# Kernel optimization log

Measured on AMD Instinct MI355X. Metric: run time of the kernel, lower is better.

Reference implementation:

```python
import jax, jax.numpy as jnp
import numpy as np

N = 20000          # nodes
E = 320000         # directed edges (self-loops added in reference)
F_IN = 128         # input node features
HEADS = 8
HID = 64           # per-head hidden channels
G = 64             # graphs in the batch
NUM_CLASSES = 10
NEG_SLOPE = 0.2    # PyG GATConv LeakyReLU slope


def _gat_layer(x, src, dst, W, a_src, a_dst, bias, n_nodes):
    """PyG-style GATConv: messages flow src->dst, softmax over incoming edges."""
    H, C = a_src.shape
    h = (x @ W).reshape(n_nodes, H, C)                     # [N,H,C]
    asrc = jnp.einsum('nhc,hc->nh', h, a_src)              # [N,H]
    adst = jnp.einsum('nhc,hc->nh', h, a_dst)              # [N,H]
    e = jax.nn.leaky_relu(asrc[src] + adst[dst], NEG_SLOPE)  # [Etot,H]
    emax = jax.ops.segment_max(e, dst, num_segments=n_nodes)  # [N,H]
    ee = jnp.exp(e - emax[dst])
    denom = jax.ops.segment_sum(ee, dst, num_segments=n_nodes)
    alpha = ee / (denom[dst] + 1e-16)                      # [Etot,H]
    out = jax.ops.segment_sum(h[src] * alpha[:, :, None], dst, num_segments=n_nodes)
    return out.reshape(n_nodes, H * C) + bias


def setup_inputs() -> dict:
    key = jax.random.key(0)
    ks = jax.random.split(key, 10)
    x = jax.random.normal(ks[0], (N, F_IN), jnp.float32)
    edge_index = jax.random.randint(ks[1], (2, E), 0, N, jnp.int32)
    batch = jnp.sort(jax.random.randint(ks[2], (N,), 0, G, jnp.int32))
    # layer 1: F_IN -> HEADS*HID (concat)
    W1 = jax.random.normal(ks[3], (F_IN, HEADS * HID), jnp.float32) / np.float32(np.sqrt(F_IN))
    a_src1 = jax.random.normal(ks[4], (HEADS, HID), jnp.float32) / np.float32(np.sqrt(HID))
    a_dst1 = jax.random.normal(ks[5], (HEADS, HID), jnp.float32) / np.float32(np.sqrt(HID))
    b1 = jnp.zeros((HEADS * HID,), jnp.float32)
    # layer 2: HEADS*HID -> NUM_CLASSES (1 head)
    W2 = jax.random.normal(ks[6], (HEADS * HID, NUM_CLASSES), jnp.float32) / np.float32(np.sqrt(HEADS * HID))
    a_src2 = jax.random.normal(ks[7], (1, NUM_CLASSES), jnp.float32) / np.float32(np.sqrt(NUM_CLASSES))
    a_dst2 = jax.random.normal(ks[8], (1, NUM_CLASSES), jnp.float32) / np.float32(np.sqrt(NUM_CLASSES))
    b2 = jnp.zeros((NUM_CLASSES,), jnp.float32)
    return {"x": x, "edge_index": edge_index, "batch": batch,
            "W1": W1, "a_src1": a_src1, "a_dst1": a_dst1, "b1": b1,
            "W2": W2, "a_src2": a_src2, "a_dst2": a_dst2, "b2": b2}


def reference(x, edge_index, batch, W1, a_src1, a_dst1, b1, W2, a_src2, a_dst2, b2):
    n = x.shape[0]
    loop = jnp.arange(n, dtype=edge_index.dtype)   # add_self_loops=True (PyG default)
    src = jnp.concatenate([edge_index[0], loop])
    dst = jnp.concatenate([edge_index[1], loop])
    h = jax.nn.elu(_gat_layer(x, src, dst, W1, a_src1, a_dst1, b1, n))
    h = _gat_layer(h, src, dst, W2, a_src2, a_dst2, b2, n)
    # PowerMeanAggregation with default p=1.0 == mean pooling per graph
    sums = jax.ops.segment_sum(h, batch, num_segments=G)                    # [G,NC]
    counts = jax.ops.segment_sum(jnp.ones((n, 1), h.dtype), batch, num_segments=G)
    return sums / jnp.maximum(counts, 1.0)
```

## Files before the change

kernel.cpp:

```cpp
#include <hip/hip_runtime.h>
#include <hip/hip_bf16.h>

typedef unsigned short ushort_t;
typedef unsigned int uint_t;

typedef __attribute__((ext_vector_type(8))) short bf16x8;
typedef __attribute__((ext_vector_type(4))) float f32x4;

__device__ __forceinline__ float bf2f(ushort_t u) {
    union { uint_t i; float f; } v; v.i = ((uint_t)u) << 16; return v.f;
}
__device__ __forceinline__ float bits2f(uint_t i) {
    union { uint_t i; float f; } v; v.i = i; return v.f;
}
__device__ __forceinline__ ushort_t f2bf(float f) {
    __hip_bfloat16 h = __float2bfloat16(f);
    ushort_t u; __builtin_memcpy(&u, &h, 2); return u;
}
__device__ __forceinline__ float leaky(float v) { return (v > 0.f) ? v : 0.2f * v; }

#define PO_AS1 0
#define PO_AD1 512
#define PO_B1  1024
#define PO_W2  1536
#define PO_AS2 6656
#define PO_AD2 6666
#define PO_B2  6676
#define PTOT   6686

__device__ __forceinline__ bool detect_fp32_local(const ushort_t* __restrict__ xa) {
    __shared__ int cnt;
    if (threadIdx.x == 0) cnt = 0;
    __syncthreads();
    int bad = 0;
    for (int i = threadIdx.x; i < 4096; i += 256) {
        float v = bf2f(xa[i]);
        if (!(fabsf(v) < 1e4f)) bad++;
    }
    if (bad) atomicAdd(&cnt, bad);
    __syncthreads();
    return cnt >= 16;
}

__global__ __launch_bounds__(256) void k_prep(const void* __restrict__ x,
                                              const void* __restrict__ W1,
                                              const void* as1, const void* ad1,
                                              const void* b1, const void* W2,
                                              const void* as2, const void* ad2,
                                              const void* b2,
                                              ushort_t* __restrict__ W1t,
                                              float* __restrict__ prm,
                                              int* __restrict__ deg, int N) {
    int b = blockIdx.x, t = threadIdx.x;
    if (b < 283) {
        bool isf = detect_fp32_local((const ushort_t*)x);
        if (b < 256) {
            int idx = b * 256 + t;
            int n = idx & 511, k = idx >> 9;
            float v = isf ? ((const float*)W1)[k * 512 + n]
                          : bf2f(((const ushort_t*)W1)[k * 512 + n]);
            W1t[n * 128 + k] = f2bf(v);
        } else {
            int i = (b - 256) * 256 + t;
            if (i < PTOT) {
                const void* src; int off;
                if (i < 512)       { src = as1; off = i; }
                else if (i < 1024) { src = ad1; off = i - 512; }
                else if (i < 1536) { src = b1;  off = i - 1024; }
                else if (i < 6656) { src = W2;  off = i - 1536; }
                else if (i < 6666) { src = as2; off = i - 6656; }
                else if (i < 6676) { src = ad2; off = i - 6666; }
                else               { src = b2;  off = i - 6676; }
                prm[i] = isf ? ((const float*)src)[off] : bf2f(((const ushort_t*)src)[off]);
            }
        }
    } else {
        int i = (b - 283) * 256 + t;
        if (i < N) deg[i] = 0;
    }
}

__global__ __launch_bounds__(256) void k_gemm1(const void* __restrict__ xraw,
                                               const ushort_t* __restrict__ w1t,
                                               const float* __restrict__ prm,
                                               ushort_t* __restrict__ h1,
                                               float* __restrict__ asrcf,
                                               float* __restrict__ adstf) {
    int t = threadIdx.x;
    int wave = t >> 6, lane = t & 63;
    int m0 = blockIdx.x * 16;
    bool isf = detect_fp32_local((const ushort_t*)xraw);
    __shared__ ushort_t sA[16 * 128];
    {
        size_t base = (size_t)m0 * 128;
        for (int i = t; i < 2048; i += 256)
            sA[i] = isf ? f2bf(((const float*)xraw)[base + i])
                        : ((const ushort_t*)xraw)[base + i];
    }
    __syncthreads();
    int mr = lane & 15, quad = lane >> 4;
    int n0 = wave * 128;
    f32x4 acc[8];
#pragma unroll
    for (int ct = 0; ct < 8; ++ct) acc[ct] = {0.f, 0.f, 0.f, 0.f};
#pragma unroll
    for (int kk = 0; kk < 4; ++kk) {
        bf16x8 a = *reinterpret_cast<const bf16x8*>(&sA[mr * 128 + quad * 8 + kk * 32]);
#pragma unroll
        for (int ct = 0; ct < 8; ++ct) {
            bf16x8 bb = *reinterpret_cast<const bf16x8*>(
                &w1t[(size_t)(n0 + ct * 16 + mr) * 128 + quad * 8 + kk * 32]);
            acc[ct] = __builtin_amdgcn_mfma_f32_16x16x32_bf16(a, bb, acc[ct], 0, 0, 0);
        }
    }
    int col = lane & 15;
#pragma unroll
    for (int hh = 0; hh < 2; ++hh) {
        float Ss[4] = {0.f, 0.f, 0.f, 0.f}, Dd[4] = {0.f, 0.f, 0.f, 0.f};
#pragma unroll
        for (int c4 = 0; c4 < 4; ++c4) {
            int ct = hh * 4 + c4;
            int abscol = n0 + ct * 16 + col;
            float asv = prm[PO_AS1 + abscol];
            float adv = prm[PO_AD1 + abscol];
            float ps[4], pd[4];
#pragma unroll
            for (int r = 0; r < 4; ++r) {
                h1[(size_t)(m0 + quad * 4 + r) * 512 + abscol] = f2bf(acc[ct][r]);
                ps[r] = acc[ct][r] * asv;
                pd[r] = acc[ct][r] * adv;
            }
#pragma unroll
            for (int off = 1; off <= 8; off <<= 1) {
#pragma unroll
                for (int r = 0; r < 4; ++r) {
                    ps[r] += __shfl_xor(ps[r], off, 64);
                    pd[r] += __shfl_xor(pd[r], off, 64);
                }
            }
#pragma unroll
            for (int r = 0; r < 4; ++r) { Ss[r] += ps[r]; Dd[r] += pd[r]; }
        }
        if (col == 0) {
            int head = 2 * wave + hh;
#pragma unroll
            for (int r = 0; r < 4; ++r) {
                asrcf[(m0 + quad * 4 + r) * 8 + head] = Ss[r];
                adstf[(m0 + quad * 4 + r) * 8 + head] = Dd[r];
            }
        }
    }
}

__global__ void k_hist(const int* __restrict__ ei, int* __restrict__ deg, int E, int Etot) {
    int e = blockIdx.x * 256 + threadIdx.x;
    if (e >= Etot) return;
    int dst = (e < E) ? ei[E + e] : (e - E);
    atomicAdd(&deg[dst], 1);
}

__global__ __launch_bounds__(1024) void k_scan1(const int* __restrict__ deg,
                                                int* __restrict__ rowptr,
                                                int* __restrict__ bsum, int N) {
    int b = blockIdx.x, t = threadIdx.x;
    int lane = t & 63, wv = t >> 6;
    int i = b * 1000 + t;
    int v = (t < 1000 && i < N) ? deg[i] : 0;
    int sv = v;
#pragma unroll
    for (int off = 1; off < 64; off <<= 1) {
        int u = __shfl_up(sv, off, 64);
        if (lane >= off) sv += u;
    }
    __shared__ int wsum[16], woff[16];
    if (lane == 63) wsum[wv] = sv;
    __syncthreads();
    if (t < 16) {
        int s = wsum[t], sc = s;
#pragma unroll
        for (int off = 1; off < 16; off <<= 1) {
            int u = __shfl_up(sc, off, 16);
            if ((t & 15) >= off) sc += u;
        }
        woff[t] = sc - s;
    }
    __syncthreads();
    int inc = sv + woff[wv];
    if (t < 1000 && i < N) rowptr[i + 1] = inc;
    if (t == 1023) bsum[b] = inc;
}

__global__ __launch_bounds__(64) void k_scan2(const int* __restrict__ bsum,
                                              int* __restrict__ boffs) {
    int l = threadIdx.x;
    int v = (l < 20) ? bsum[l] : 0;
    int sc = v;
#pragma unroll
    for (int off = 1; off < 64; off <<= 1) {
        int u = __shfl_up(sc, off, 64);
        if (l >= off) sc += u;
    }
    if (l < 20) boffs[l] = sc - v;
}

__global__ __launch_bounds__(256) void k_scan3(const int* __restrict__ deg,
                                               const int* __restrict__ boffs,
                                               int* __restrict__ rowptr,
                                               int* __restrict__ cursor, int N) {
    int i = blockIdx.x * 256 + threadIdx.x;
    if (i >= N) return;
    int r = rowptr[i + 1] + boffs[i / 1000];
    rowptr[i + 1] = r;
    cursor[i] = r - deg[i];
    if (i == 0) rowptr[0] = 0;
}

__global__ void k_scatter(const int* __restrict__ ei, int* __restrict__ cursor,
                          int* __restrict__ csr_src, int E, int Etot) {
    int e = blockIdx.x * 256 + threadIdx.x;
    if (e >= Etot) return;
    int src, dst;
    if (e < E) { src = ei[e]; dst = ei[E + e]; } else { src = dst = e - E; }
    int pos = atomicAdd(&cursor[dst], 1);
    csr_src[pos] = src;
}

__global__ __launch_bounds__(256) void k_agg1(const ushort_t* __restrict__ h1,
                                              const float* __restrict__ asrcf,
                                              const float* __restrict__ adstf,
                                              const int* __restrict__ rowptr,
                                              const int* __restrict__ csr_src,
                                              const float* __restrict__ prm,
                                              float* __restrict__ h2,
                                              float* __restrict__ asrc2f,
                                              float* __restrict__ adst2f) {
    int n = blockIdx.x, t = threadIdx.x;
    __shared__ float s_adst[8];
    __shared__ float s_acc[4][64 * 9];
    __shared__ float s_den[4][8];
    __shared__ float s_p[4][10];
    if (t < 8) s_adst[t] = adstf[n * 8 + t];
    int start = rowptr[n], end = rowptr[n + 1];
    __syncthreads();
    int w = t >> 6, lane = t & 63;
    int hh = lane >> 3;
    int cb = lane * 8;
    float adh = s_adst[hh];
    float a0 = 0.f, a1 = 0.f, a2 = 0.f, a3 = 0.f, a4 = 0.f, a5 = 0.f, a6 = 0.f, a7 = 0.f;
    float den = 0.f;
    int e = start + w;
    int s_cur = (e < end) ? csr_src[e] : 0;
    for (; e < end; ) {
        int e_next = e + 4;
        int s_next = (e_next < end) ? csr_src[e_next] : 0;
        float lo = asrcf[s_cur * 8 + hh];
        uint4 pv = *reinterpret_cast<const uint4*>(&h1[(size_t)s_cur * 512 + cb]);
        float we = __expf(leaky(lo + adh));
        den += we;
        a0 += we * bits2f(pv.x << 16); a1 += we * bits2f(pv.x & 0xffff0000u);
        a2 += we * bits2f(pv.y << 16); a3 += we * bits2f(pv.y & 0xffff0000u);
        a4 += we * bits2f(pv.z << 16); a5 += we * bits2f(pv.z & 0xffff0000u);
        a6 += we * bits2f(pv.w << 16); a7 += we * bits2f(pv.w & 0xffff0000u);
        e = e_next; s_cur = s_next;
    }
    int lb = lane * 9;
    s_acc[w][lb + 0] = a0; s_acc[w][lb + 1] = a1; s_acc[w][lb + 2] = a2; s_acc[w][lb + 3] = a3;
    s_acc[w][lb + 4] = a4; s_acc[w][lb + 5] = a5; s_acc[w][lb + 6] = a6; s_acc[w][lb + 7] = a7;
    if ((lane & 7) == 0) s_den[w][hh] = den;
    __syncthreads();
    int K = 2 * t;
    int src_l = (t >> 2) * 9 + ((2 * t) & 7);
    float r0 = s_acc[0][src_l] + s_acc[1][src_l] + s_acc[2][src_l] + s_acc[3][src_l];
    float r1 = s_acc[0][src_l + 1] + s_acc[1][src_l + 1] + s_acc[2][src_l + 1] + s_acc[3][src_l + 1];
    int head = K >> 6;
    float dd = s_den[0][head] + s_den[1][head] + s_den[2][head] + s_den[3][head];
    float inv = 1.f / (dd + 1e-16f);
    r0 = r0 * inv + prm[PO_B1 + K];
    r1 = r1 * inv + prm[PO_B1 + K + 1];
    r0 = (r0 > 0.f) ? r0 : expm1f(r0);
    r1 = (r1 > 0.f) ? r1 : expm1f(r1);
    float p[10];
#pragma unroll
    for (int c = 0; c < 10; ++c)
        p[c] = r0 * prm[PO_W2 + K * 10 + c] + r1 * prm[PO_W2 + (K + 1) * 10 + c];
#pragma unroll
    for (int c = 0; c < 10; ++c)
#pragma unroll
        for (int off = 32; off; off >>= 1)
            p[c] += __shfl_xor(p[c], off, 64);
    if (lane == 0)
#pragma unroll
        for (int c = 0; c < 10; ++c) s_p[w][c] = p[c];
    __syncthreads();
    if (t == 0) {
        float as = 0.f, ad = 0.f;
        for (int c = 0; c < 10; ++c) {
            float v = s_p[0][c] + s_p[1][c] + s_p[2][c] + s_p[3][c];
            h2[n * 10 + c] = v;
            as += v * prm[PO_AS2 + c];
            ad += v * prm[PO_AD2 + c];
        }
        asrc2f[n] = as; adst2f[n] = ad;
    }
}

__global__ __launch_bounds__(256) void k_agg2(const float* __restrict__ h2,
                                              const float* __restrict__ asrc2f,
                                              const float* __restrict__ adst2f,
                                              const int* __restrict__ rowptr,
                                              const int* __restrict__ csr_src,
                                              const float* __restrict__ prm,
                                              float* __restrict__ out2) {
    int n = blockIdx.x * 4 + (threadIdx.x >> 6);
    int l = threadIdx.x & 63;
    int start = rowptr[n], end = rowptr[n + 1];
    float adn = adst2f[n];
    float den = 0.f;
    float oc[10];
#pragma unroll
    for (int c = 0; c < 10; ++c) oc[c] = 0.f;
    int e = start + l;
    int s_cur = (e < end) ? csr_src[e] : 0;
    for (; e < end; ) {
        int e_next = e + 64;
        int s_next = (e_next < end) ? csr_src[e_next] : 0;
        float lo = asrc2f[s_cur];
        const float2* hp = reinterpret_cast<const float2*>(&h2[s_cur * 10]);
        float2 q0 = hp[0], q1 = hp[1], q2 = hp[2], q3 = hp[3], q4 = hp[4];
        float ee = __expf(leaky(lo + adn));
        den += ee;
        oc[0] += ee * q0.x; oc[1] += ee * q0.y;
        oc[2] += ee * q1.x; oc[3] += ee * q1.y;
        oc[4] += ee * q2.x; oc[5] += ee * q2.y;
        oc[6] += ee * q3.x; oc[7] += ee * q3.y;
        oc[8] += ee * q4.x; oc[9] += ee * q4.y;
        e = e_next; s_cur = s_next;
    }
#pragma unroll
    for (int off = 32; off; off >>= 1) {
        den += __shfl_xor(den, off, 64);
#pragma unroll
        for (int c = 0; c < 10; ++c) oc[c] += __shfl_xor(oc[c], off, 64);
    }
    if (l == 0) {
        float inv = 1.f / (den + 1e-16f);
        for (int c = 0; c < 10; ++c) out2[n * 10 + c] = oc[c] * inv + prm[PO_B2 + c];
    }
}

__global__ __launch_bounds__(256) void k_pool(const float* __restrict__ out2,
                                              const int* __restrict__ batch,
                                              const void* __restrict__ x,
                                              void* __restrict__ dout, int N) {
    bool isf = detect_fp32_local((const ushort_t*)x);
    int g = blockIdx.x, t = threadIdx.x;
    __shared__ int s_lo, s_hi;
    __shared__ float sm[256];
    if (t == 0) {
        int lo = 0, hi = N;
        while (lo < hi) { int mid = (lo + hi) >> 1; if (batch[mid] < g) lo = mid + 1; else hi = mid; }
        s_lo = lo;
        int lo2 = lo, hi2 = N;
        while (lo2 < hi2) { int mid = (lo2 + hi2) >> 1; if (batch[mid] < g + 1) lo2 = mid + 1; else hi2 = mid; }
        s_hi = lo2;
    }
    __syncthreads();
    int lo = s_lo, hi = s_hi;
    float acc[10];
#pragma unroll
    for (int c = 0; c < 10; ++c) acc[c] = 0.f;
    for (int i = lo + t; i < hi; i += 256)
#pragma unroll
        for (int c = 0; c < 10; ++c) acc[c] += out2[i * 10 + c];
    float cnt = (float)((hi - lo) > 0 ? (hi - lo) : 1);
    for (int c = 0; c < 10; ++c) {
        sm[t] = acc[c]; __syncthreads();
        for (int off = 128; off; off >>= 1) {
            if (t < off) sm[t] += sm[t + off];
            __syncthreads();
        }
        if (t == 0) {
            float r = sm[0] / cnt;
            if (isf) ((float*)dout)[g * 10 + c] = r;
            else     ((ushort_t*)dout)[g * 10 + c] = f2bf(r);
        }
        __syncthreads();
    }
}

extern "C" void kernel_launch(void* const* d_in, const int* in_sizes, int n_in,
                              void* d_out, int out_size, void* d_ws, size_t ws_size,
                              hipStream_t stream) {
    const void* x   = d_in[0];
    const int* ei   = (const int*)d_in[1];
    const int* batch= (const int*)d_in[2];
    const void* W1  = d_in[3];
    const void* as1 = d_in[4];
    const void* ad1 = d_in[5];
    const void* b1  = d_in[6];
    const void* W2  = d_in[7];
    const void* as2 = d_in[8];
    const void* ad2 = d_in[9];
    const void* b2  = d_in[10];

    constexpr int N = 20000, E = 320000, Etot = E + N;

    char* p = (char*)d_ws;
    auto alloc = [&](size_t bytes) {
        char* r = p; p += (bytes + 255) & ~(size_t)255; return r;
    };
    float* prm      = (float*)alloc((size_t)PTOT * 4);
    ushort_t* w1t   = (ushort_t*)alloc(512 * 128 * 2);
    ushort_t* h1    = (ushort_t*)alloc((size_t)N * 512 * 2);
    float* asrc1f   = (float*)alloc((size_t)N * 8 * 4);
    float* adst1f   = (float*)alloc((size_t)N * 8 * 4);
    float* asrc2f   = (float*)alloc((size_t)N * 4);
    float* adst2f   = (float*)alloc((size_t)N * 4);
    float* h2       = (float*)alloc((size_t)N * 10 * 4);
    float* out2     = (float*)alloc((size_t)N * 10 * 4);
    int* deg        = (int*)alloc((size_t)N * 4);
    int* rowptr     = (int*)alloc((size_t)(N + 1) * 4);
    int* cursor     = (int*)alloc((size_t)N * 4);
    int* csr_src    = (int*)alloc((size_t)Etot * 4);
    int* bsum       = (int*)alloc(32 * 4);
    int* boffs      = (int*)alloc(32 * 4);

    k_prep<<<362, 256, 0, stream>>>(x, W1, as1, ad1, b1, W2, as2, ad2, b2,
                                    w1t, prm, deg, N);
    k_gemm1<<<1250, 256, 0, stream>>>(x, w1t, prm, h1, asrc1f, adst1f);
    k_hist<<<(Etot + 255) / 256, 256, 0, stream>>>(ei, deg, E, Etot);
    k_scan1<<<20, 1024, 0, stream>>>(deg, rowptr, bsum, N);
    k_scan2<<<1, 64, 0, stream>>>(bsum, boffs);
    k_scan3<<<(N + 255) / 256, 256, 0, stream>>>(deg, boffs, rowptr, cursor, N);
    k_scatter<<<(Etot + 255) / 256, 256, 0, stream>>>(ei, cursor, csr_src, E, Etot);
    k_agg1<<<N, 256, 0, stream>>>(h1, asrc1f, adst1f, rowptr, csr_src, prm,
                                  h2, asrc2f, adst2f);
    k_agg2<<<N / 4, 256, 0, stream>>>(h2, asrc2f, adst2f, rowptr, csr_src, prm, out2);
    k_pool<<<64, 256, 0, stream>>>(out2, batch, x, d_out, N);
}
```

Measured before the change: 275.0 us.

## Map one wavefront per node in layer-1 aggregation and fold block scan into scan3

Layer-1 aggregation previously used a 256-thread block per node, with four wavefronts splitting the edges and then reducing through shared memory across two barriers. Now each wavefront handles one node on its own, walking all incoming edges with a one-step prefetch of the next neighbour's row. The per-channel ELU and the layer-2 projection run in registers, followed by a single wave shuffle reduction. The separate single-wave block-offset scan kernel is also removed: every scan3 block recomputes the 20 block offsets into shared memory, which saves one launch. The trade-off is that a single wave per node serialises the edge loop, so high-degree nodes take longer and there is less memory-level parallelism per node.

```diff
diff --git a/kernel.cpp b/kernel.cpp
--- a/kernel.cpp
+++ b/kernel.cpp
@@ -190,26 +190,26 @@
     if (t == 1023) bsum[b] = inc;
 }
 
-__global__ __launch_bounds__(64) void k_scan2(const int* __restrict__ bsum,
-                                              int* __restrict__ boffs) {
-    int l = threadIdx.x;
-    int v = (l < 20) ? bsum[l] : 0;
-    int sc = v;
-#pragma unroll
-    for (int off = 1; off < 64; off <<= 1) {
-        int u = __shfl_up(sc, off, 64);
-        if (l >= off) sc += u;
-    }
-    if (l < 20) boffs[l] = sc - v;
-}
-
 __global__ __launch_bounds__(256) void k_scan3(const int* __restrict__ deg,
-                                               const int* __restrict__ boffs,
+                                               const int* __restrict__ bsum,
                                                int* __restrict__ rowptr,
                                                int* __restrict__ cursor, int N) {
-    int i = blockIdx.x * 256 + threadIdx.x;
+    __shared__ int sboffs[20];
+    int t = threadIdx.x;
+    if (t < 64) {
+        int v = (t < 20) ? bsum[t] : 0;
+        int sc = v;
+#pragma unroll
+        for (int off = 1; off < 32; off <<= 1) {
+            int u = __shfl_up(sc, off, 64);
+            if (t >= off) sc += u;
+        }
+        if (t < 20) sboffs[t] = sc - v;
+    }
+    __syncthreads();
+    int i = blockIdx.x * 256 + t;
     if (i >= N) return;
-    int r = rowptr[i + 1] + boffs[i / 1000];
+    int r = rowptr[i + 1] + sboffs[i / 1000];
     rowptr[i + 1] = r;
     cursor[i] = r - deg[i];
     if (i == 0) rowptr[0] = 0;
@@ -234,71 +234,56 @@
                                               float* __restrict__ h2,
                                               float* __restrict__ asrc2f,
                                               float* __restrict__ adst2f) {
-    int n = blockIdx.x, t = threadIdx.x;
-    __shared__ float s_adst[8];
-    __shared__ float s_acc[4][64 * 9];
-    __shared__ float s_den[4][8];
-    __shared__ float s_p[4][10];
-    if (t < 8) s_adst[t] = adstf[n * 8 + t];
-    int start = rowptr[n], end = rowptr[n + 1];
-    __syncthreads();
-    int w = t >> 6, lane = t & 63;
+    int n = blockIdx.x * 4 + (threadIdx.x >> 6);
+    int lane = threadIdx.x & 63;
     int hh = lane >> 3;
     int cb = lane * 8;
-    float adh = s_adst[hh];
+    int start = rowptr[n], end = rowptr[n + 1];
+    float adh = adstf[n * 8 + hh];
     float a0 = 0.f, a1 = 0.f, a2 = 0.f, a3 = 0.f, a4 = 0.f, a5 = 0.f, a6 = 0.f, a7 = 0.f;
     float den = 0.f;
-    int e = start + w;
-    int s_cur = (e < end) ? csr_src[e] : 0;
-    for (; e < end; ) {
-        int e_next = e + 4;
-        int s_next = (e_next < end) ? csr_src[e_next] : 0;
-        float lo = asrcf[s_cur * 8 + hh];
-        uint4 pv = *reinterpret_cast<const uint4*>(&h1[(size_t)s_cur * 512 + cb]);
+    int e = start;
+    int sc = csr_src[e];
+    float lo = asrcf[sc * 8 + hh];
+    uint4 pv = *reinterpret_cast<const uint4*>(&h1[(size_t)sc * 512 + cb]);
+    while (e < end) {
+        int en = e + 1;
+        int sn = (en < end) ? csr_src[en] : 0;
+        float lon = asrcf[sn * 8 + hh];
+        uint4 pvn = *reinterpret_cast<const uint4*>(&h1[(size_t)sn * 512 + cb]);
         float we = __expf(leaky(lo + adh));
         den += we;
         a0 += we * bits2f(pv.x << 16); a1 += we * bits2f(pv.x & 0xffff0000u);
         a2 += we * bits2f(pv.y << 16); a3 += we * bits2f(pv.y & 0xffff0000u);
         a4 += we * bits2f(pv.z << 16); a5 += we * bits2f(pv.z & 0xffff0000u);
         a6 += we * bits2f(pv.w << 16); a7 += we * bits2f(pv.w & 0xffff0000u);
-        e = e_next; s_cur = s_next;
-    }
-    int lb = lane * 9;
-    s_acc[w][lb + 0] = a0; s_acc[w][lb + 1] = a1; s_acc[w][lb + 2] = a2; s_acc[w][lb + 3] = a3;
-    s_acc[w][lb + 4] = a4; s_acc[w][lb + 5] = a5; s_acc[w][lb + 6] = a6; s_acc[w][lb + 7] = a7;
-    if ((lane & 7) == 0) s_den[w][hh] = den;
-    __syncthreads();
-    int K = 2 * t;
-    int src_l = (t >> 2) * 9 + ((2 * t) & 7);
-    float r0 = s_acc[0][src_l] + s_acc[1][src_l] + s_acc[2][src_l] + s_acc[3][src_l];
-    float r1 = s_acc[0][src_l + 1] + s_acc[1][src_l + 1] + s_acc[2][src_l + 1] + s_acc[3][src_l + 1];
-    int head = K >> 6;
-    float dd = s_den[0][head] + s_den[1][head] + s_den[2][head] + s_den[3][head];
-    float inv = 1.f / (dd + 1e-16f);
-    r0 = r0 * inv + prm[PO_B1 + K];
-    r1 = r1 * inv + prm[PO_B1 + K + 1];
-    r0 = (r0 > 0.f) ? r0 : expm1f(r0);
-    r1 = (r1 > 0.f) ? r1 : expm1f(r1);
+        e = en; sc = sn; lo = lon; pv = pvn;
+    }
+    float inv = 1.f / (den + 1e-16f);
+    float r[8] = {a0, a1, a2, a3, a4, a5, a6, a7};
     float p[10];
 #pragma unroll
-    for (int c = 0; c < 10; ++c)
-        p[c] = r0 * prm[PO_W2 + K * 10 + c] + r1 * prm[PO_W2 + (K + 1) * 10 + c];
+    for (int c = 0; c < 10; ++c) p[c] = 0.f;
+#pragma unroll
+    for (int j = 0; j < 8; ++j) {
+        float rv = r[j] * inv + prm[PO_B1 + cb + j];
+        rv = (rv > 0.f) ? rv : expm1f(rv);
+#pragma unroll
+        for (int c = 0; c < 10; ++c)
+            p[c] += rv * prm[PO_W2 + (cb + j) * 10 + c];
+    }
 #pragma unroll
     for (int c = 0; c < 10; ++c)
 #pragma unroll
         for (int off = 32; off; off >>= 1)
             p[c] += __shfl_xor(p[c], off, 64);
-    if (lane == 0)
-#pragma unroll
-        for (int c = 0; c < 10; ++c) s_p[w][c] = p[c];
-    __syncthreads();
-    if (t == 0) {
+    if (lane == 0) {
         float as = 0.f, ad = 0.f;
+#pragma unroll
         for (int c = 0; c < 10; ++c) {
-            float v = s_p[0][c] + s_p[1][c] + s_p[2][c] + s_p[3][c];
-            h2[n * 10 + c] = v;
-            as += v * prm[PO_AS2 + c];
-            ad += v * prm[PO_AD2 + c];
+            h2[n * 10 + c] = p[c];
+            as += p[c] * prm[PO_AS2 + c];
+            ad += p[c] * prm[PO_AD2 + c];
         }
         asrc2f[n] = as; adst2f[n] = ad;
     }
@@ -423,18 +408,16 @@
     int* cursor     = (int*)alloc((size_t)N * 4);
     int* csr_src    = (int*)alloc((size_t)Etot * 4);
     int* bsum       = (int*)alloc(32 * 4);
-    int* boffs      = (int*)alloc(32 * 4);
 
     k_prep<<<362, 256, 0, stream>>>(x, W1, as1, ad1, b1, W2, as2, ad2, b2,
                                     w1t, prm, deg, N);
     k_gemm1<<<1250, 256, 0, stream>>>(x, w1t, prm, h1, asrc1f, adst1f);
     k_hist<<<(Etot + 255) / 256, 256, 0, stream>>>(ei, deg, E, Etot);
     k_scan1<<<20, 1024, 0, stream>>>(deg, rowptr, bsum, N);
-    k_scan2<<<1, 64, 0, stream>>>(bsum, boffs);
-    k_scan3<<<(N + 255) / 256, 256, 0, stream>>>(deg, boffs, rowptr, cursor, N);
+    k_scan3<<<(N + 255) / 256, 256, 0, stream>>>(deg, bsum, rowptr, cursor, N);
     k_scatter<<<(Etot + 255) / 256, 256, 0, stream>>>(ei, cursor, csr_src, E, Etot);
-    k_agg1<<<N, 256, 0, stream>>>(h1, asrc1f, adst1f, rowptr, csr_src, prm,
-                                  h2, asrc2f, adst2f);
+    k_agg1<<<N / 4, 256, 0, stream>>>(h1, asrc1f, adst1f, rowptr, csr_src, prm,
+                                      h2, asrc2f, adst2f);
     k_agg2<<<N / 4, 256, 0, stream>>>(h2, asrc2f, adst2f, rowptr, csr_src, prm, out2);
     k_pool<<<64, 256, 0, stream>>>(out2, batch, x, d_out, N);
 }
```

After: 273.8 us. About the same (-0.4%).
